# Kernel tuning notes

Measured on AMD Instinct MI355X. Metric: run time of the kernel, lower is better.

## Reference

```python
import jax, jax.numpy as jnp
import numpy as np

B_, S, D_IN, D_OUT, N_ADP, R = 4, 4096, 2048, 2048, 4, 16
SCALE = 32.0 / 16.0  # lora_alpha / r, use_rslora=False, same for all adaptors


def setup_inputs() -> dict:
    key = jax.random.key(0)
    ks = jax.random.split(key, 6)
    x = jax.random.normal(ks[0], (B_, S, D_IN), dtype=jnp.float32)
    mask = jax.random.uniform(ks[1], (N_ADP, B_, S, 1), dtype=jnp.float32)
    W = jax.random.normal(ks[2], (D_OUT, D_IN), dtype=jnp.float32) * 0.02
    b = jnp.zeros((D_OUT,), dtype=jnp.float32)
    A = jax.random.normal(ks[3], (N_ADP, R, D_IN), dtype=jnp.float32) * 0.02
    Bw = jax.random.normal(ks[4], (N_ADP, D_OUT, R), dtype=jnp.float32) * 0.02
    return {"x": x, "mask": mask, "W": W, "b": b, "A": A, "Bw": Bw}


def reference(x, mask, W, b, A, Bw):
    # base_layer: y = x @ W^T + b  -> [B, S, D_OUT]
    result = jnp.einsum('bsd,od->bso', x, W) + b
    # all adaptors batched: h = lora_A(x) -> [N, B, S, R]
    h = jnp.einsum('bsd,nrd->nbsr', x, A)
    # delta = lora_B(h) -> [N, B, S, D_OUT]
    delta = jnp.einsum('nbsr,nor->nbso', h, Bw)
    # scale, per-adaptor mask multiply, accumulate into residual
    result = result + jnp.sum(delta * SCALE * mask, axis=0)
    return result
```

## Files before the change

kernel.cpp:

```cpp
#include <hip/hip_runtime.h>
#include <stdint.h>


typedef __attribute__((ext_vector_type(8))) short bf16x8;
typedef __attribute__((ext_vector_type(4))) float f32x4;
typedef __attribute__((ext_vector_type(4))) unsigned short u16x4;
typedef __attribute__((ext_vector_type(8))) unsigned short u16x8;

#define GAS __attribute__((address_space(1)))
#define LAS __attribute__((address_space(3)))

static constexpr int BB   = 4;
static constexpr int SS   = 4096;
static constexpr int DIN  = 2048;
static constexpr int DOUT = 2048;
static constexpr int NADP = 4;
static constexpr int RR   = 16;
static constexpr int M    = BB * SS;
static constexpr int KA   = DIN + NADP * RR;
static constexpr float SCALE = 2.0f;

static_assert(KA % 64 == 0, "K-loop needs BK=64 divisibility");

__device__ __forceinline__ unsigned short f2bf(float f) {
  union { float f; uint32_t u; } v; v.f = f;
  uint32_t u = v.u;
  return (unsigned short)((u + 0x7FFFu + ((u >> 16) & 1u)) >> 16);
}

__global__ __launch_bounds__(256) void pass1_xcvt_h(
    const float* __restrict__ x, const float* __restrict__ A,
    const float* __restrict__ mask, unsigned short* __restrict__ Xaug)
{
  __shared__ unsigned short xb[64 * 64];
  __shared__ unsigned short ab[64 * 64];

  const int tid = threadIdx.x;
  const int rowBase = blockIdx.x * 64;
  const int w = tid >> 6, lane = tid & 63;
  const int quad = lane >> 4, m16 = lane & 15;

  f32x4 acc[4];
  #pragma unroll
  for (int j = 0; j < 4; ++j) acc[j] = f32x4{0.f, 0.f, 0.f, 0.f};

  for (int kc = 0; kc < DIN; kc += 64) {
    __syncthreads();
    #pragma unroll
    for (int l = 0; l < 4; ++l) {
      int v = l * 256 + tid;
      int r = v >> 4;
      int k = (v & 15) * 4;
      float4 xv = *(const float4*)(x + (size_t)(rowBase + r) * DIN + kc + k);
      u16x4 xq = { f2bf(xv.x), f2bf(xv.y), f2bf(xv.z), f2bf(xv.w) };
      *(u16x4*)(xb + r * 64 + k) = xq;
      *(u16x4*)(Xaug + (size_t)(rowBase + r) * KA + kc + k) = xq;
      float4 av = *(const float4*)(A + (size_t)r * DIN + kc + k);
      u16x4 aq = { f2bf(av.x), f2bf(av.y), f2bf(av.z), f2bf(av.w) };
      *(u16x4*)(ab + r * 64 + k) = aq;
    }
    __syncthreads();
    #pragma unroll
    for (int s = 0; s < 2; ++s) {
      bf16x8 af = *(const bf16x8*)(xb + (w * 16 + m16) * 64 + s * 32 + quad * 8);
      #pragma unroll
      for (int jt = 0; jt < 4; ++jt) {
        bf16x8 bfg = *(const bf16x8*)(ab + (jt * 16 + m16) * 64 + s * 32 + quad * 8);
        acc[jt] = __builtin_amdgcn_mfma_f32_16x16x32_bf16(af, bfg, acc[jt], 0, 0, 0);
      }
    }
  }

  const int grow0 = rowBase + w * 16 + quad * 4;
  #pragma unroll
  for (int jt = 0; jt < 4; ++jt) {
    #pragma unroll
    for (int r = 0; r < 4; ++r) {
      int grow = grow0 + r;
      float h = acc[jt][r] * mask[(size_t)jt * M + grow];
      Xaug[(size_t)grow * KA + DIN + jt * 16 + m16] = f2bf(h);
    }
  }
}

__global__ __launch_bounds__(256) void pass2_wcvt(
    const float* __restrict__ W, const float* __restrict__ Bw,
    unsigned short* __restrict__ Waug)
{
  const int idx = blockIdx.x * 256 + threadIdx.x;
  const int row = idx >> 8;
  const int k   = (idx & 255) * 8;
  float4 a = *(const float4*)(W + (size_t)row * DIN + k);
  float4 b = *(const float4*)(W + (size_t)row * DIN + k + 4);
  u16x8 q = { f2bf(a.x), f2bf(a.y), f2bf(a.z), f2bf(a.w),
              f2bf(b.x), f2bf(b.y), f2bf(b.z), f2bf(b.w) };
  *(u16x8*)(Waug + (size_t)row * KA + k) = q;

  if (idx < DOUT * NADP) {
    const int col = idx >> 2, n = idx & 3;
    const float* src = Bw + (size_t)n * DOUT * RR + (size_t)col * RR;
    #pragma unroll
    for (int t = 0; t < 4; ++t) {
      float4 bv = *(const float4*)(src + 4 * t);
      u16x4 qq = { f2bf(SCALE * bv.x), f2bf(SCALE * bv.y),
                   f2bf(SCALE * bv.z), f2bf(SCALE * bv.w) };
      *(u16x4*)(Waug + (size_t)col * KA + DIN + n * 16 + 4 * t) = qq;
    }
  }
}

__global__ __launch_bounds__(256, 3) void gemm_aug(
    const unsigned short* __restrict__ Xa, const unsigned short* __restrict__ Wa,
    const float* __restrict__ bias, float* __restrict__ out)
{
  __shared__ unsigned short lds_a[128 * 64];
  __shared__ unsigned short lds_b[128 * 64];

  const int tid = threadIdx.x;
  const int bn = blockIdx.x, bm = blockIdx.y;
  const int w = tid >> 6, lane = tid & 63;
  const int wm = w >> 1, wn = w & 1;
  const int quad = lane >> 4, m16 = lane & 15;

  f32x4 acc[4][4];
  #pragma unroll
  for (int i = 0; i < 4; ++i)
    #pragma unroll
    for (int j = 0; j < 4; ++j) acc[i][j] = f32x4{0.f, 0.f, 0.f, 0.f};

  const unsigned short* ga = Xa + (size_t)bm * 128 * KA;
  const unsigned short* gb = Wa + (size_t)bn * 128 * KA;

  size_t goff[4];
  int ldso[4];
  #pragma unroll
  for (int l = 0; l < 4; ++l) {
    int p = l * 256 + tid;
    int r = p >> 3;
    int c = (p & 7) ^ (r & 7);
    goff[l] = (size_t)r * KA + c * 8;
    ldso[l] = (l * 256 + (tid & ~63)) * 8;
  }

  for (int k0 = 0; k0 < KA; k0 += 64) {
    __syncthreads();
    #pragma unroll
    for (int l = 0; l < 4; ++l) {
      __builtin_amdgcn_global_load_lds((const GAS void*)(ga + goff[l] + k0),
                                       (LAS void*)(lds_a + ldso[l]), 16, 0, 0);
      __builtin_amdgcn_global_load_lds((const GAS void*)(gb + goff[l] + k0),
                                       (LAS void*)(lds_b + ldso[l]), 16, 0, 0);
    }
    __syncthreads();

    #pragma unroll
    for (int s = 0; s < 2; ++s) {
      const int cc = ((s * 4 + quad) ^ (m16 & 7)) * 8;
      bf16x8 af[4], bfg[4];
      #pragma unroll
      for (int i = 0; i < 4; ++i)
        af[i] = *(const bf16x8*)(lds_a + (wm * 64 + i * 16 + m16) * 64 + cc);
      #pragma unroll
      for (int j = 0; j < 4; ++j)
        bfg[j] = *(const bf16x8*)(lds_b + (wn * 64 + j * 16 + m16) * 64 + cc);
      #pragma unroll
      for (int i = 0; i < 4; ++i)
        #pragma unroll
        for (int j = 0; j < 4; ++j)
          acc[i][j] = __builtin_amdgcn_mfma_f32_16x16x32_bf16(af[i], bfg[j],
                                                              acc[i][j], 0, 0, 0);
    }
  }

  float bv[4];
  #pragma unroll
  for (int j = 0; j < 4; ++j) bv[j] = bias[bn * 128 + wn * 64 + j * 16 + m16];
  #pragma unroll
  for (int i = 0; i < 4; ++i) {
    const int row0 = bm * 128 + wm * 64 + i * 16 + quad * 4;
    #pragma unroll
    for (int j = 0; j < 4; ++j) {
      const int col = bn * 128 + wn * 64 + j * 16 + m16;
      #pragma unroll
      for (int r = 0; r < 4; ++r)
        out[(size_t)(row0 + r) * DOUT + col] = acc[i][j][r] + bv[j];
    }
  }
}

extern "C" void kernel_launch(void* const* d_in, const int* in_sizes, int n_in,
                              void* d_out, int out_size, void* d_ws, size_t ws_size,
                              hipStream_t stream) {
  const float* x    = (const float*)d_in[0];
  const float* mask = (const float*)d_in[1];
  const float* W    = (const float*)d_in[2];
  const float* bias = (const float*)d_in[3];
  const float* A    = (const float*)d_in[4];
  const float* Bw   = (const float*)d_in[5];
  float* out = (float*)d_out;

  unsigned short* Xaug = (unsigned short*)d_ws;
  unsigned short* Waug = Xaug + (size_t)M * KA;

  pass1_xcvt_h<<<dim3(M / 64), dim3(256), 0, stream>>>(x, A, mask, Xaug);
  pass2_wcvt<<<dim3((DOUT * (DIN / 8)) / 256), dim3(256), 0, stream>>>(W, Bw, Waug);
  gemm_aug<<<dim3(DOUT / 128, M / 128), dim3(256), 0, stream>>>(Xaug, Waug, bias, out);
}
```

Baseline: 474.7 us.

## Split-K the LoRA-A projection pass and add a separate reduce-and-mask kernel

The x-conversion plus LoRA-A projection pass is split four ways along K, so it launches four times as many blocks (1024 instead of 256) and each block walks a quarter of the reduction. Partial h sums are written as fp32 to a workspace buffer. A new small kernel then sums the partials, applies the mask and writes bf16 into the augmented X. This is meant to raise occupancy across the many CUs in the first pass, at the cost of an extra launch and extra partial-sum traffic.

Measured after the change: 401.7 us. -15.4%, faster.

```diff
diff --git a/kernel.cpp b/kernel.cpp
--- a/kernel.cpp
+++ b/kernel.cpp
@@ -20,6 +20,9 @@
 static constexpr int KA   = DIN + NADP * RR;
 static constexpr float SCALE = 2.0f;
 
+static constexpr int KSPLIT = 4;
+static constexpr int KCH    = DIN / KSPLIT;
+
 static_assert(KA % 64 == 0, "K-loop needs BK=64 divisibility");
 
 __device__ __forceinline__ unsigned short f2bf(float f) {
@@ -28,15 +31,18 @@
   return (unsigned short)((u + 0x7FFFu + ((u >> 16) & 1u)) >> 16);
 }
 
-__global__ __launch_bounds__(256) void pass1_xcvt_h(
+__global__ __launch_bounds__(256) void pass1a_conv_hpart(
     const float* __restrict__ x, const float* __restrict__ A,
-    const float* __restrict__ mask, unsigned short* __restrict__ Xaug)
+    unsigned short* __restrict__ Xaug, float* __restrict__ Hpart)
 {
   __shared__ unsigned short xb[64 * 64];
   __shared__ unsigned short ab[64 * 64];
 
   const int tid = threadIdx.x;
-  const int rowBase = blockIdx.x * 64;
+  const int rb = blockIdx.x >> 2;
+  const int ks = blockIdx.x & 3;
+  const int rowBase = rb * 64;
+  const int kBase = ks * KCH;
   const int w = tid >> 6, lane = tid & 63;
   const int quad = lane >> 4, m16 = lane & 15;
 
@@ -44,7 +50,7 @@
   #pragma unroll
   for (int j = 0; j < 4; ++j) acc[j] = f32x4{0.f, 0.f, 0.f, 0.f};
 
-  for (int kc = 0; kc < DIN; kc += 64) {
+  for (int kc = kBase; kc < kBase + KCH; kc += 64) {
     __syncthreads();
     #pragma unroll
     for (int l = 0; l < 4; ++l) {
@@ -77,10 +83,24 @@
     #pragma unroll
     for (int r = 0; r < 4; ++r) {
       int grow = grow0 + r;
-      float h = acc[jt][r] * mask[(size_t)jt * M + grow];
-      Xaug[(size_t)grow * KA + DIN + jt * 16 + m16] = f2bf(h);
-    }
-  }
+      Hpart[(((size_t)ks * M + grow) << 6) + jt * 16 + m16] = acc[jt][r];
+    }
+  }
+}
+
+__global__ __launch_bounds__(256) void pass1b_reduce_mask(
+    const float* __restrict__ Hpart, const float* __restrict__ mask,
+    unsigned short* __restrict__ Xaug)
+{
+  const int idx = blockIdx.x * 256 + threadIdx.x;
+  const int row = idx >> 6;
+  const int j   = idx & 63;
+  float s = 0.f;
+  #pragma unroll
+  for (int ks = 0; ks < KSPLIT; ++ks)
+    s += Hpart[(((size_t)ks * M) << 6) + idx];
+  s *= mask[(size_t)(j >> 4) * M + row];
+  Xaug[(size_t)row * KA + DIN + j] = f2bf(s);
 }
 
 __global__ __launch_bounds__(256) void pass2_wcvt(
@@ -201,8 +221,10 @@
 
   unsigned short* Xaug = (unsigned short*)d_ws;
   unsigned short* Waug = Xaug + (size_t)M * KA;
-
-  pass1_xcvt_h<<<dim3(M / 64), dim3(256), 0, stream>>>(x, A, mask, Xaug);
+  float* Hpart = (float*)(Waug + (size_t)DOUT * KA);
+
+  pass1a_conv_hpart<<<dim3(M / 64 * KSPLIT), dim3(256), 0, stream>>>(x, A, Xaug, Hpart);
+  pass1b_reduce_mask<<<dim3(M * 64 / 256), dim3(256), 0, stream>>>(Hpart, mask, Xaug);
   pass2_wcvt<<<dim3((DOUT * (DIN / 8)) / 256), dim3(256), 0, stream>>>(W, Bw, Waug);
   gemm_aug<<<dim3(DOUT / 128, M / 128), dim3(256), 0, stream>>>(Xaug, Waug, bias, out);
 }
```
